# Kernel tuning notes

Hardware: AMD Instinct MI355X
Metric: run time of the kernel (lower is better)

## Reference

```python
import jax, jax.numpy as jnp
import numpy as np

B, S, D, H = 64, 512, 1024, 1024

def setup_inputs() -> dict:
    key = jax.random.key(0)
    ks = jax.random.split(key, 7)
    s = 1.0 / np.sqrt(H)
    return {
        "x": jax.random.normal(ks[0], (B, S, D), dtype=jnp.float32),
        "h0": jax.random.normal(ks[1], (H,), dtype=jnp.float32),
        "c0": jax.random.normal(ks[2], (H,), dtype=jnp.float32),
        "Wi": jax.random.normal(ks[3], (4 * H, D), dtype=jnp.float32) * s,
        "bi": jax.random.normal(ks[4], (4 * H,), dtype=jnp.float32) * s,
        "Wh": jax.random.normal(ks[5], (4 * H, H), dtype=jnp.float32) * s,
        "bh": jax.random.normal(ks[6], (4 * H,), dtype=jnp.float32) * s,
    }

def reference(x, h0, c0, Wi, bi, Wh, bh):
    # x: [B,S,D]; h0,c0: [H] broadcast over batch (matches torch zeros(H) semantics)
    b, _, _ = x.shape
    h = jnp.broadcast_to(h0, (b, H))
    c = jnp.broadcast_to(c0, (b, H))
    # Precompute the input projection for all timesteps in one big GEMM (same math).
    xg = jnp.einsum('bsd,gd->bsg', x, Wi) + bi  # [B,S,4H]

    def step(carry, xg_t):
        h, c = carry
        gates = xg_t + h @ Wh.T + bh  # [B,4H]
        i = jax.nn.sigmoid(gates[:, :H])
        f = jax.nn.sigmoid(gates[:, H:2 * H])
        g = jnp.tanh(gates[:, 2 * H:3 * H])
        o = jax.nn.sigmoid(gates[:, 3 * H:])
        c = f * c + i * g
        h = o * jnp.tanh(c)
        return (h, c), h

    (h, c), hs = jax.lax.scan(step, (h, c), jnp.swapaxes(xg, 0, 1))  # hs: [S,B,H]
    hidden_seq = jnp.swapaxes(hs, 0, 1)  # [B,S,H]
    return hidden_seq, (h, c)
```

## Files before the change

kernel.cpp:

```cpp
#include <hip/hip_runtime.h>
#include <cstdint>
#include <cstddef>

#define B_ 64
#define S_ 512
#define D_ 1024
#define H_ 1024
#define G_ 4096
#define NBLK 256

typedef short short8 __attribute__((ext_vector_type(8)));
typedef float floatx4 __attribute__((ext_vector_type(4)));

__device__ __forceinline__ unsigned short bf16_rne(float f) {
  union { float f; unsigned u; } v; v.f = f;
  return (unsigned short)((v.u + 0x7FFFu + ((v.u >> 16) & 1u)) >> 16);
}
__device__ __forceinline__ float sigf(float x) { return 1.0f / (1.0f + __expf(-x)); }
__device__ __forceinline__ float tanhf_fast(float x) {
  float e = __expf(2.0f * x);
  return 1.0f - 2.0f / (e + 1.0f);
}

__device__ __forceinline__ void astore64(void* p, uint64_t v) {
  __hip_atomic_store((unsigned long long*)p, (unsigned long long)v,
                     __ATOMIC_RELAXED, __HIP_MEMORY_SCOPE_AGENT);
}
__device__ __forceinline__ void astore32(unsigned* p, unsigned v) {
  __hip_atomic_store(p, v, __ATOMIC_RELAXED, __HIP_MEMORY_SCOPE_AGENT);
}
__device__ __forceinline__ unsigned aload32(const unsigned* p) {
  return __hip_atomic_load(p, __ATOMIC_RELAXED, __HIP_MEMORY_SCOPE_AGENT);
}
__device__ __forceinline__ void cload2x128(uint4* d0, uint4* d1, const void* p0, const void* p1) {
  asm volatile("global_load_dwordx4 %0, %2, off sc0 sc1\n\t"
               "global_load_dwordx4 %1, %3, off sc0 sc1\n\t"
               "s_waitcnt vmcnt(0)"
               : "=&v"(*d0), "=&v"(*d1)
               : "v"(p0), "v"(p1)
               : "memory");
}

__global__ void f32_to_bf16_k(const float* __restrict__ s, unsigned short* __restrict__ d, int n) {
  int i = (blockIdx.x * 256 + threadIdx.x) * 4;
  if (i < n) {
    float4 v = *(const float4*)(s + i);
    ushort4 o;
    o.x = bf16_rne(v.x); o.y = bf16_rne(v.y); o.z = bf16_rne(v.z); o.w = bf16_rne(v.w);
    *(ushort4*)(d + i) = o;
  }
}

__global__ void bsum_k(const float* __restrict__ bi, const float* __restrict__ bh, float* __restrict__ o) {
  int i = blockIdx.x * 256 + threadIdx.x;
  if (i < G_) o[i] = bi[i] + bh[i];
}

__global__ void hinit_k(const float* __restrict__ h0, unsigned short* __restrict__ hb) {
  int i = blockIdx.x * 256 + threadIdx.x;
  if (i < B_ * H_) hb[i] = bf16_rne(h0[i & (H_ - 1)]);
}

__global__ __launch_bounds__(256, 3) void gemm_xg(
    const unsigned short* __restrict__ xa,
    const unsigned short* __restrict__ wb,
    const float* __restrict__ bsum,
    void* __restrict__ xgv, int xg16)
{
  __shared__ unsigned short As[128 * 72];
  __shared__ unsigned short Bs[128 * 72];
  const int tid = threadIdx.x, ln = tid & 63, wv = tid >> 6;
  const int q = ln >> 4, lr = ln & 15;
  const int bid = blockIdx.x;
  const int nt = bid & 31, mt = bid >> 5;
  const int m0 = mt << 7, n0 = nt << 7;
  const int wm = (wv & 1) << 6, wn = (wv >> 1) << 6;
  floatx4 acc[4][4] = {};

  for (int kk = 0; kk < 1024; kk += 64) {
    __syncthreads();
#pragma unroll
    for (int i = 0; i < 4; i++) {
      int f = i * 256 + tid;
      int row = f >> 3, c8 = (f & 7) << 3;
      short8 va = *(const short8*)(xa + (size_t)(m0 + row) * 1024 + kk + c8);
      short8 vb = *(const short8*)(wb + (size_t)(n0 + row) * 1024 + kk + c8);
      *(short8*)(As + row * 72 + c8) = va;
      *(short8*)(Bs + row * 72 + c8) = vb;
    }
    __syncthreads();
#pragma unroll
    for (int ks = 0; ks < 2; ks++) {
      short8 af[4], bf[4];
#pragma unroll
      for (int mi = 0; mi < 4; mi++)
        af[mi] = *(const short8*)(As + (wm + mi * 16 + lr) * 72 + ks * 32 + q * 8);
#pragma unroll
      for (int ni = 0; ni < 4; ni++)
        bf[ni] = *(const short8*)(Bs + (wn + ni * 16 + lr) * 72 + ks * 32 + q * 8);
#pragma unroll
      for (int mi = 0; mi < 4; mi++)
#pragma unroll
        for (int ni = 0; ni < 4; ni++)
          acc[mi][ni] = __builtin_amdgcn_mfma_f32_16x16x32_bf16(af[mi], bf[ni], acc[mi][ni], 0, 0, 0);
    }
  }
  const int b = m0 >> 9, s0 = m0 & 511;
#pragma unroll
  for (int mi = 0; mi < 4; mi++) {
#pragma unroll
    for (int r = 0; r < 4; r++) {
      int mrow = wm + mi * 16 + q * 4 + r;
      size_t base = (size_t)(s0 + mrow) * (B_ * G_) + (size_t)b * G_;
#pragma unroll
      for (int ni = 0; ni < 4; ni++) {
        int n = n0 + wn + ni * 16 + lr;
        float v = acc[mi][ni][r] + bsum[n];
        if (xg16) ((unsigned short*)xgv)[base + n] = bf16_rne(v);
        else      ((float*)xgv)[base + n] = v;
      }
    }
  }
}

__global__ __launch_bounds__(1024, 1) void lstm_rec(
    const void* __restrict__ xgv, int xg16,
    const unsigned short* __restrict__ wh,
    unsigned short* __restrict__ hb,
    const float* __restrict__ c0,
    float* __restrict__ out_hid,
    float* __restrict__ out_h,
    float* __restrict__ out_c,
    unsigned* __restrict__ sync)
{
  __shared__ unsigned short hs[16 * 1032];
  __shared__ float red[3][4][16][16];
  __shared__ unsigned short hout_bf[256];
  __shared__ float hout_f[256];

  const int tid = threadIdx.x, ln = tid & 63, wv = tid >> 6;
  const int nt = wv & 3, kt = wv >> 2;
  const int bid = blockIdx.x, bg = bid & 3, cg = bid >> 2;
  const int r0 = bg << 4, j0 = cg << 4;
  const int nloc = ln & 15, q = ln >> 4;
  const int tg = nloc >> 2, u = nloc & 3;
  const int j = j0 + (nt << 2) + u;
  const int gcol = tg * 1024 + j;

  unsigned* arr_bg = sync + (bg << 6);
  unsigned* flag_bg = sync + 256 + (bg << 7);

  short8 bfr[8];
#pragma unroll
  for (int s8 = 0; s8 < 8; s8++)
    bfr[s8] = *(const short8*)(wh + (size_t)gcol * 1024 + kt * 256 + s8 * 32 + q * 8);

  float cst[4];
#pragma unroll
  for (int r = 0; r < 4; r++) cst[r] = c0[j];

  for (int t = 0; t < 512; t++) {
    const unsigned short* hr = hb + (t & 1) * (B_ * H_);
    unsigned short* hw = hb + ((t + 1) & 1) * (B_ * H_);

    float xv[4] = {0.f, 0.f, 0.f, 0.f};
    if (kt == 0) {
      const size_t xbase = (size_t)t * (B_ * G_) + (size_t)r0 * G_ + gcol;
      if (xg16) {
#pragma unroll
        for (int r = 0; r < 4; r++) {
          unsigned short w = ((const unsigned short*)xgv)[xbase + (size_t)(q * 4 + r) * G_];
          union { unsigned uu; float ff; } cv; cv.uu = ((unsigned)w) << 16; xv[r] = cv.ff;
        }
      } else {
#pragma unroll
        for (int r = 0; r < 4; r++)
          xv[r] = ((const float*)xgv)[xbase + (size_t)(q * 4 + r) * G_];
      }
    }

    {
      int g0 = tid, g1 = tid + 1024;
      const void* p0 = hr + ((r0 + (g0 >> 7)) << 10) + ((g0 & 127) << 3);
      const void* p1 = hr + ((r0 + (g1 >> 7)) << 10) + ((g1 & 127) << 3);
      uint4 a, b;
      cload2x128(&a, &b, p0, p1);
      *(uint4*)(hs + (g0 >> 7) * 1032 + ((g0 & 127) << 3)) = a;
      *(uint4*)(hs + (g1 >> 7) * 1032 + ((g1 & 127) << 3)) = b;
    }
    __syncthreads();

    floatx4 acc = {0.f, 0.f, 0.f, 0.f};
#pragma unroll
    for (int s8 = 0; s8 < 8; s8++) {
      short8 af = *(const short8*)(hs + nloc * 1032 + kt * 256 + s8 * 32 + q * 8);
      acc = __builtin_amdgcn_mfma_f32_16x16x32_bf16(af, bfr[s8], acc, 0, 0, 0);
    }
    if (kt) {
#pragma unroll
      for (int r = 0; r < 4; r++) red[kt - 1][nt][q * 4 + r][nloc] = acc[r];
    }
    __syncthreads();

    if (kt == 0) {
      float gv[4];
#pragma unroll
      for (int r = 0; r < 4; r++)
        gv[r] = acc[r] + red[0][nt][q * 4 + r][nloc] + red[1][nt][q * 4 + r][nloc]
              + red[2][nt][q * 4 + r][nloc] + xv[r];
      const int sb = q << 4;
#pragma unroll
      for (int r = 0; r < 4; r++) {
        float vi = __shfl(gv[r], sb + u);
        float vf = __shfl(gv[r], sb + 4 + u);
        float vg = __shfl(gv[r], sb + 8 + u);
        float vo = __shfl(gv[r], sb + 12 + u);
        float i_ = sigf(vi), f_ = sigf(vf), g_ = tanhf_fast(vg), o_ = sigf(vo);
        float cn = f_ * cst[r] + i_ * g_;
        cst[r] = cn;
        float hn = o_ * tanhf_fast(cn);
        if (tg == 0) {
          int m = (q << 2) + r;
          hout_bf[(m << 4) + (nt << 2) + u] = bf16_rne(hn);
          hout_f [(m << 4) + (nt << 2) + u] = hn;
          if (t == 511) {
            int brow = r0 + m;
            out_h[(brow << 10) + j] = hn;
            out_c[(brow << 10) + j] = cn;
          }
        }
      }
    }
    __syncthreads();

    if (wv == 0) {
      int row = ln >> 2, c4 = (ln & 3) << 2;
      uint64_t hv = *(const uint64_t*)(hout_bf + (row << 4) + c4);
      astore64(hw + ((r0 + row) << 10) + j0 + c4, hv);
      __asm__ volatile("" ::: "memory");
      __builtin_amdgcn_s_waitcnt(0);
      __asm__ volatile("" ::: "memory");
      if (t < 511) {
        if (ln == 0) astore32(arr_bg + cg, (unsigned)(t + 1));
        const unsigned tgt = (unsigned)(t + 1);
        if (cg == 0) {
          for (;;) {
            unsigned v = aload32(arr_bg + ln);
#pragma unroll
            for (int d = 32; d >= 1; d >>= 1) {
              unsigned o = __shfl_xor(v, d);
              v = v < o ? v : o;
            }
            if (v >= tgt) break;
            __builtin_amdgcn_s_sleep(2);
          }
          if (ln < 8) astore32(flag_bg + (ln << 4), tgt);
        } else if (ln == 0) {
          const unsigned* fl = flag_bg + ((cg & 7) << 4);
          while (aload32(fl) < tgt) __builtin_amdgcn_s_sleep(8);
        }
      }
    } else if (wv == 1) {
      int row = ln >> 2, c4 = (ln & 3) << 2;
      float4 fv = *(const float4*)(hout_f + (row << 4) + c4);
      *(float4*)(out_hid + (size_t)(r0 + row) * (S_ * H_) + (size_t)t * H_ + j0 + c4) = fv;
    }
    __syncthreads();
  }
}

extern "C" void kernel_launch(void* const* d_in, const int* in_sizes, int n_in,
                              void* d_out, int out_size, void* d_ws, size_t ws_size,
                              hipStream_t stream) {
  const float* x  = (const float*)d_in[0];
  const float* h0 = (const float*)d_in[1];
  const float* c0 = (const float*)d_in[2];
  const float* Wi = (const float*)d_in[3];
  const float* bi = (const float*)d_in[4];
  const float* Wh = (const float*)d_in[5];
  const float* bh = (const float*)d_in[6];

  float* out_hid = (float*)d_out;
  float* out_h = out_hid + (size_t)B_ * S_ * H_;
  float* out_c = out_h + (size_t)B_ * H_;

  uint8_t* ws = (uint8_t*)d_ws;
  const size_t xg_fp32 = (size_t)S_ * B_ * G_ * 4;
  const size_t xg_bf16 = (size_t)S_ * B_ * G_ * 2;
  const size_t xbf_b = (size_t)B_ * S_ * D_ * 2;
  const size_t w_b = (size_t)G_ * D_ * 2;
  const size_t rest = xbf_b + 2 * w_b + (size_t)G_ * 4 + (size_t)2 * B_ * H_ * 2 + 8192;
  int xg16 = (ws_size >= xg_fp32 + rest) ? 0 : 1;
  size_t xg_bytes = xg16 ? xg_bf16 : xg_fp32;

  size_t off = 0;
  void* xg = (void*)(ws + off);                      off += xg_bytes;
  unsigned short* xbf = (unsigned short*)(ws + off); off += xbf_b;
  unsigned short* wib = (unsigned short*)(ws + off); off += w_b;
  unsigned short* whb = (unsigned short*)(ws + off); off += w_b;
  float* bsum = (float*)(ws + off);                  off += (size_t)G_ * 4;
  unsigned short* hb = (unsigned short*)(ws + off);  off += (size_t)2 * B_ * H_ * 2;
  off = (off + 255) & ~(size_t)255;
  unsigned* syncp = (unsigned*)(ws + off);

  hipMemsetAsync(syncp, 0, 4096, stream);
  f32_to_bf16_k<<<(B_ * S_ * D_ / 4 + 255) / 256, 256, 0, stream>>>(x, xbf, B_ * S_ * D_);
  f32_to_bf16_k<<<(G_ * D_ / 4 + 255) / 256, 256, 0, stream>>>(Wi, wib, G_ * D_);
  f32_to_bf16_k<<<(G_ * D_ / 4 + 255) / 256, 256, 0, stream>>>(Wh, whb, G_ * D_);
  bsum_k<<<G_ / 256, 256, 0, stream>>>(bi, bh, bsum);
  hinit_k<<<(B_ * H_ + 255) / 256, 256, 0, stream>>>(h0, hb);

  gemm_xg<<<dim3((S_ * B_ / 128) * (G_ / 128)), 256, 0, stream>>>(xbf, wib, bsum, xg, xg16);

  void* args[] = { (void*)&xg, (void*)&xg16, (void*)&whb, (void*)&hb, (void*)&c0,
                   (void*)&out_hid, (void*)&out_h, (void*)&out_c, (void*)&syncp };
  hipLaunchCooperativeKernel((void*)lstm_rec, dim3(NBLK), dim3(1024), args, 0, stream);
}
```

Before: 3.182 ms.

## Replace grid barrier with per-element step tags packed alongside hidden-state values

Each bf16 hidden value is stored in a 32-bit word whose low half carries the timestep tag. Consumers spin on their own 64-byte slice until every tag matches the current step. This removes the separate arrive/flag barrier, with its two-level polling and its waitcnt on stores. The cost is double the size of the h buffer and polling traffic from every thread. Correctness now relies on the 64-bit stores being seen atomically. The final syncthreads is also replaced by an LDS-only wait plus barrier.

```diff
diff --git a/kernel.cpp b/kernel.cpp
--- a/kernel.cpp
+++ b/kernel.cpp
@@ -26,20 +26,21 @@
   __hip_atomic_store((unsigned long long*)p, (unsigned long long)v,
                      __ATOMIC_RELAXED, __HIP_MEMORY_SCOPE_AGENT);
 }
-__device__ __forceinline__ void astore32(unsigned* p, unsigned v) {
-  __hip_atomic_store(p, v, __ATOMIC_RELAXED, __HIP_MEMORY_SCOPE_AGENT);
-}
-__device__ __forceinline__ unsigned aload32(const unsigned* p) {
-  return __hip_atomic_load(p, __ATOMIC_RELAXED, __HIP_MEMORY_SCOPE_AGENT);
-}
-__device__ __forceinline__ void cload2x128(uint4* d0, uint4* d1, const void* p0, const void* p1) {
-  asm volatile("global_load_dwordx4 %0, %2, off sc0 sc1\n\t"
-               "global_load_dwordx4 %1, %3, off sc0 sc1\n\t"
+__device__ __forceinline__ void cpoll64(uint4* a, uint4* b, uint4* c, uint4* d, const void* p) {
+  asm volatile("global_load_dwordx4 %0, %4, off sc0 sc1\n\t"
+               "global_load_dwordx4 %1, %4, off offset:16 sc0 sc1\n\t"
+               "global_load_dwordx4 %2, %4, off offset:32 sc0 sc1\n\t"
+               "global_load_dwordx4 %3, %4, off offset:48 sc0 sc1\n\t"
                "s_waitcnt vmcnt(0)"
-               : "=&v"(*d0), "=&v"(*d1)
-               : "v"(p0), "v"(p1)
-               : "memory");
-}
+               : "=&v"(*a), "=&v"(*b), "=&v"(*c), "=&v"(*d)
+               : "v"(p) : "memory");
+}
+
+#define BARRIER_LGKM() do {                                   \
+    asm volatile("s_waitcnt lgkmcnt(0)" ::: "memory");        \
+    __builtin_amdgcn_s_barrier();                             \
+    asm volatile("" ::: "memory");                            \
+  } while (0)
 
 __global__ void f32_to_bf16_k(const float* __restrict__ s, unsigned short* __restrict__ d, int n) {
   int i = (blockIdx.x * 256 + threadIdx.x) * 4;
@@ -56,9 +57,9 @@
   if (i < G_) o[i] = bi[i] + bh[i];
 }
 
-__global__ void hinit_k(const float* __restrict__ h0, unsigned short* __restrict__ hb) {
+__global__ void hinit_k(const float* __restrict__ h0, unsigned* __restrict__ hb32) {
   int i = blockIdx.x * 256 + threadIdx.x;
-  if (i < B_ * H_) hb[i] = bf16_rne(h0[i & (H_ - 1)]);
+  if (i < B_ * H_) hb32[i] = ((unsigned)bf16_rne(h0[i & (H_ - 1)])) << 16;
 }
 
 __global__ __launch_bounds__(256, 3) void gemm_xg(
@@ -126,12 +127,11 @@
 __global__ __launch_bounds__(1024, 1) void lstm_rec(
     const void* __restrict__ xgv, int xg16,
     const unsigned short* __restrict__ wh,
-    unsigned short* __restrict__ hb,
+    unsigned* __restrict__ hb32,
     const float* __restrict__ c0,
     float* __restrict__ out_hid,
     float* __restrict__ out_h,
-    float* __restrict__ out_c,
-    unsigned* __restrict__ sync)
+    float* __restrict__ out_c)
 {
   __shared__ unsigned short hs[16 * 1032];
   __shared__ float red[3][4][16][16];
@@ -147,9 +147,6 @@
   const int j = j0 + (nt << 2) + u;
   const int gcol = tg * 1024 + j;
 
-  unsigned* arr_bg = sync + (bg << 6);
-  unsigned* flag_bg = sync + 256 + (bg << 7);
-
   short8 bfr[8];
 #pragma unroll
   for (int s8 = 0; s8 < 8; s8++)
@@ -159,10 +156,9 @@
 #pragma unroll
   for (int r = 0; r < 4; r++) cst[r] = c0[j];
 
+  const int srow = tid >> 6, scc = (tid & 63) << 4;
+
   for (int t = 0; t < 512; t++) {
-    const unsigned short* hr = hb + (t & 1) * (B_ * H_);
-    unsigned short* hw = hb + ((t + 1) & 1) * (B_ * H_);
-
     float xv[4] = {0.f, 0.f, 0.f, 0.f};
     if (kt == 0) {
       const size_t xbase = (size_t)t * (B_ * G_) + (size_t)r0 * G_ + gcol;
@@ -180,13 +176,28 @@
     }
 
     {
-      int g0 = tid, g1 = tid + 1024;
-      const void* p0 = hr + ((r0 + (g0 >> 7)) << 10) + ((g0 & 127) << 3);
-      const void* p1 = hr + ((r0 + (g1 >> 7)) << 10) + ((g1 & 127) << 3);
-      uint4 a, b;
-      cload2x128(&a, &b, p0, p1);
-      *(uint4*)(hs + (g0 >> 7) * 1032 + ((g0 & 127) << 3)) = a;
-      *(uint4*)(hs + (g1 >> 7) * 1032 + ((g1 & 127) << 3)) = b;
+      const unsigned* hp = hb32 + (size_t)(t & 1) * (B_ * H_)
+                         + ((size_t)(r0 + srow) << 10) + scc;
+      const unsigned tg16 = (unsigned)t & 0xffffu;
+      uint4 w0, w1, w2, w3;
+      for (;;) {
+        cpoll64(&w0, &w1, &w2, &w3, hp);
+        unsigned dv = ((w0.x ^ tg16) | (w0.y ^ tg16) | (w0.z ^ tg16) | (w0.w ^ tg16)
+                     | (w1.x ^ tg16) | (w1.y ^ tg16) | (w1.z ^ tg16) | (w1.w ^ tg16)
+                     | (w2.x ^ tg16) | (w2.y ^ tg16) | (w2.z ^ tg16) | (w2.w ^ tg16)
+                     | (w3.x ^ tg16) | (w3.y ^ tg16) | (w3.z ^ tg16) | (w3.w ^ tg16)) & 0xffffu;
+        if (dv == 0) break;
+        __builtin_amdgcn_s_sleep(2);
+      }
+      unsigned* hd = (unsigned*)(hs + srow * 1032 + scc);
+      hd[0] = (w0.x >> 16) | (w0.y & 0xffff0000u);
+      hd[1] = (w0.z >> 16) | (w0.w & 0xffff0000u);
+      hd[2] = (w1.x >> 16) | (w1.y & 0xffff0000u);
+      hd[3] = (w1.z >> 16) | (w1.w & 0xffff0000u);
+      hd[4] = (w2.x >> 16) | (w2.y & 0xffff0000u);
+      hd[5] = (w2.z >> 16) | (w2.w & 0xffff0000u);
+      hd[6] = (w3.x >> 16) | (w3.y & 0xffff0000u);
+      hd[7] = (w3.z >> 16) | (w3.w & 0xffff0000u);
     }
     __syncthreads();
 
@@ -234,38 +245,25 @@
     __syncthreads();
 
     if (wv == 0) {
-      int row = ln >> 2, c4 = (ln & 3) << 2;
-      uint64_t hv = *(const uint64_t*)(hout_bf + (row << 4) + c4);
-      astore64(hw + ((r0 + row) << 10) + j0 + c4, hv);
-      __asm__ volatile("" ::: "memory");
-      __builtin_amdgcn_s_waitcnt(0);
-      __asm__ volatile("" ::: "memory");
       if (t < 511) {
-        if (ln == 0) astore32(arr_bg + cg, (unsigned)(t + 1));
-        const unsigned tgt = (unsigned)(t + 1);
-        if (cg == 0) {
-          for (;;) {
-            unsigned v = aload32(arr_bg + ln);
-#pragma unroll
-            for (int d = 32; d >= 1; d >>= 1) {
-              unsigned o = __shfl_xor(v, d);
-              v = v < o ? v : o;
-            }
-            if (v >= tgt) break;
-            __builtin_amdgcn_s_sleep(2);
-          }
-          if (ln < 8) astore32(flag_bg + (ln << 4), tgt);
-        } else if (ln == 0) {
-          const unsigned* fl = flag_bg + ((cg & 7) << 4);
-          while (aload32(fl) < tgt) __builtin_amdgcn_s_sleep(8);
-        }
+        unsigned* hw32 = hb32 + (size_t)((t + 1) & 1) * (B_ * H_);
+        const int row = ln >> 2, c4 = (ln & 3) << 2;
+        const uint64_t tag = (unsigned)(t + 1);
+        const unsigned short* hb4 = hout_bf + (row << 4) + c4;
+        uint64_t w01 = ((((uint64_t)hb4[0] << 16) | tag))
+                     | ((((uint64_t)hb4[1] << 16) | tag) << 32);
+        uint64_t w23 = ((((uint64_t)hb4[2] << 16) | tag))
+                     | ((((uint64_t)hb4[3] << 16) | tag) << 32);
+        unsigned* dst = hw32 + ((size_t)(r0 + row) << 10) + j0 + c4;
+        astore64(dst, w01);
+        astore64(dst + 2, w23);
       }
     } else if (wv == 1) {
       int row = ln >> 2, c4 = (ln & 3) << 2;
       float4 fv = *(const float4*)(hout_f + (row << 4) + c4);
       *(float4*)(out_hid + (size_t)(r0 + row) * (S_ * H_) + (size_t)t * H_ + j0 + c4) = fv;
     }
-    __syncthreads();
+    BARRIER_LGKM();
   }
 }
 
@@ -289,7 +287,8 @@
   const size_t xg_bf16 = (size_t)S_ * B_ * G_ * 2;
   const size_t xbf_b = (size_t)B_ * S_ * D_ * 2;
   const size_t w_b = (size_t)G_ * D_ * 2;
-  const size_t rest = xbf_b + 2 * w_b + (size_t)G_ * 4 + (size_t)2 * B_ * H_ * 2 + 8192;
+  const size_t hb_b = (size_t)2 * B_ * H_ * 4;
+  const size_t rest = xbf_b + 2 * w_b + (size_t)G_ * 4 + hb_b + 8192;
   int xg16 = (ws_size >= xg_fp32 + rest) ? 0 : 1;
   size_t xg_bytes = xg16 ? xg_bf16 : xg_fp32;
 
@@ -299,20 +298,18 @@
   unsigned short* wib = (unsigned short*)(ws + off); off += w_b;
   unsigned short* whb = (unsigned short*)(ws + off); off += w_b;
   float* bsum = (float*)(ws + off);                  off += (size_t)G_ * 4;
-  unsigned short* hb = (unsigned short*)(ws + off);  off += (size_t)2 * B_ * H_ * 2;
-  off = (off + 255) & ~(size_t)255;
-  unsigned* syncp = (unsigned*)(ws + off);
-
-  hipMemsetAsync(syncp, 0, 4096, stream);
+  unsigned* hb32 = (unsigned*)(ws + off);            off += hb_b;
+
+  hipMemsetAsync(hb32, 0xFF, hb_b, stream);
   f32_to_bf16_k<<<(B_ * S_ * D_ / 4 + 255) / 256, 256, 0, stream>>>(x, xbf, B_ * S_ * D_);
   f32_to_bf16_k<<<(G_ * D_ / 4 + 255) / 256, 256, 0, stream>>>(Wi, wib, G_ * D_);
   f32_to_bf16_k<<<(G_ * D_ / 4 + 255) / 256, 256, 0, stream>>>(Wh, whb, G_ * D_);
   bsum_k<<<G_ / 256, 256, 0, stream>>>(bi, bh, bsum);
-  hinit_k<<<(B_ * H_ + 255) / 256, 256, 0, stream>>>(h0, hb);
+  hinit_k<<<(B_ * H_ + 255) / 256, 256, 0, stream>>>(h0, hb32);
 
   gemm_xg<<<dim3((S_ * B_ / 128) * (G_ / 128)), 256, 0, stream>>>(xbf, wib, bsum, xg, xg16);
 
-  void* args[] = { (void*)&xg, (void*)&xg16, (void*)&whb, (void*)&hb, (void*)&c0,
-                   (void*)&out_hid, (void*)&out_h, (void*)&out_c, (void*)&syncp };
+  void* args[] = { (void*)&xg, (void*)&xg16, (void*)&whb, (void*)&hb32, (void*)&c0,
+                   (void*)&out_hid, (void*)&out_h, (void*)&out_c };
   hipLaunchCooperativeKernel((void*)lstm_rec, dim3(NBLK), dim3(1024), args, 0, stream);
 }
```

After: 3.445 ms. 8.2% more time.
